# Performance work log

Hardware: AMD Instinct MI355X
Metric: run time of the kernel (lower is better)

Reference implementation:

```python
import jax, jax.numpy as jnp
import numpy as np

B, C, H, W = 2, 512, 64, 64
NUM_GROUPS = 32
EPS = 1e-6


def setup_inputs() -> dict:
    key = jax.random.key(0)
    ks = jax.random.split(key, 6)
    s = 1.0 / np.sqrt(C)
    return {
        "x": jax.random.normal(ks[0], (B, C, H, W), dtype=jnp.float32),
        "gn_scale": jnp.ones((C,), jnp.float32),
        "gn_bias": jnp.zeros((C,), jnp.float32),
        "wq": jax.random.normal(ks[1], (C, C), jnp.float32) * s,
        "bq": jnp.zeros((C,), jnp.float32),
        "wk": jax.random.normal(ks[2], (C, C), jnp.float32) * s,
        "bk": jnp.zeros((C,), jnp.float32),
        "wv": jax.random.normal(ks[3], (C, C), jnp.float32) * s,
        "bv": jnp.zeros((C,), jnp.float32),
        "wp": jax.random.normal(ks[4], (C, C), jnp.float32) * s,
        "bp": jnp.zeros((C,), jnp.float32),
    }


def group_norm(x, scale, bias):
    # x: [b, c, h, w]; GroupNorm with NUM_GROUPS groups, eps=1e-6, affine
    b, c, h, w = x.shape
    xg = x.reshape(b, NUM_GROUPS, c // NUM_GROUPS, h, w)
    mean = jnp.mean(xg, axis=(2, 3, 4), keepdims=True)
    var = jnp.var(xg, axis=(2, 3, 4), keepdims=True)
    xg = (xg - mean) * jax.lax.rsqrt(var + EPS)
    xn = xg.reshape(b, c, h, w)
    return xn * scale[None, :, None, None] + bias[None, :, None, None]


def reference(x, gn_scale, gn_bias, wq, bq, wk, bk, wv, bv, wp, bp):
    b, c, h, w = x.shape
    n = h * w
    hn = group_norm(x, gn_scale, gn_bias).reshape(b, c, n)  # [b,c,n]
    # 1x1 convs == per-pixel linear over channels
    q = jnp.einsum('dc,bcn->bdn', wq, hn) + bq[None, :, None]
    k = jnp.einsum('dc,bcn->bdn', wk, hn) + bk[None, :, None]
    v = jnp.einsum('dc,bcn->bdn', wv, hn) + bv[None, :, None]
    # attn[b,i,j] = softmax_j( q[:, :, i] . k[:, :, j] / sqrt(c) )
    attn = jnp.einsum('bci,bcj->bij', q, k) * (float(c) ** -0.5)
    attn = jax.nn.softmax(attn, axis=-1)
    out = jnp.einsum('bcj,bij->bci', v, attn)  # [b,c,n]
    out = jnp.einsum('dc,bcn->bdn', wp, out) + bp[None, :, None]
    return x + out.reshape(b, c, h, w)
```

## Files before the change

### kernel.cpp

```cpp
#include <hip/hip_runtime.h>

typedef __bf16 bf16x8 __attribute__((ext_vector_type(8)));
typedef float f32x4 __attribute__((ext_vector_type(4)));
typedef int i32x8 __attribute__((ext_vector_type(8)));
typedef _Float16 h8 __attribute__((ext_vector_type(8)));


#if defined(__has_builtin)
#if __has_builtin(__builtin_amdgcn_global_load_lds)
#define HAS_GLL 1
#endif
#endif

__device__ __forceinline__ void async_copy16(const void* g, void* l) {
#ifdef HAS_GLL
    __builtin_amdgcn_global_load_lds(
        (const __attribute__((address_space(1))) unsigned int*)g,
        (__attribute__((address_space(3))) unsigned int*)l, 16, 0, 0);
#else
    *(int4*)l = *(const int4*)g;
#endif
}

__device__ __forceinline__ unsigned char to_fp8(float v) {
    return (unsigned char)(__builtin_amdgcn_cvt_pk_fp8_f32(v, v, 0, false) & 0xFF);
}

#define MXSCALE 0x7F7F7F7F

__global__ __launch_bounds__(256) void gn_partial_kernel(const float* __restrict__ x,
                                                         float* __restrict__ ps) {
    int blk = blockIdx.x;
    const float4* base = (const float4*)x + (size_t)blk * 1024;
    float s1 = 0.f, s2 = 0.f;
#pragma unroll
    for (int i = 0; i < 4; ++i) {
        float4 v = base[threadIdx.x + (i << 8)];
        s1 += v.x + v.y + v.z + v.w;
        s2 += v.x * v.x + v.y * v.y + v.z * v.z + v.w * v.w;
    }
    for (int off = 32; off >= 1; off >>= 1) {
        s1 += __shfl_xor(s1, off);
        s2 += __shfl_xor(s2, off);
    }
    __shared__ float r1[4], r2[4];
    int wave = threadIdx.x >> 6, lane = threadIdx.x & 63;
    if (lane == 0) { r1[wave] = s1; r2[wave] = s2; }
    __syncthreads();
    if (threadIdx.x == 0) {
        ps[blk] = r1[0] + r1[1] + r1[2] + r1[3];
        ps[1024 + blk] = r2[0] + r2[1] + r2[2] + r2[3];
    }
}

__global__ __launch_bounds__(256) void gn_apply_kernel(const float* __restrict__ x,
                                                       const float* __restrict__ gn_scale,
                                                       const float* __restrict__ gn_bias,
                                                       const float* __restrict__ ps,
                                                       __bf16* __restrict__ hn_t) {
    __shared__ float tile[32][33];
    int b = blockIdx.z;
    int n0 = blockIdx.x * 32, c0 = blockIdx.y * 32;
    int tx = threadIdx.x & 31, ty = threadIdx.x >> 5;
    const float* xb = x + (size_t)b * 512 * 4096;
#pragma unroll
    for (int r = 0; r < 4; ++r) {
        int c = ty + r * 8;
        tile[c][tx] = xb[(size_t)(c0 + c) * 4096 + n0 + tx];
    }
    int c = c0 + tx;
    int g = (b << 5) + (c >> 4);
    float s1 = 0.f, s2 = 0.f;
#pragma unroll
    for (int i = 0; i < 16; ++i) {
        s1 += ps[(g << 4) + i];
        s2 += ps[1024 + (g << 4) + i];
    }
    float m = s1 * (1.f / 65536.f);
    float var = s2 * (1.f / 65536.f) - m * m;
    float rs = rsqrtf(var + 1e-6f);
    float sc = gn_scale[c] * rs;
    float bi = gn_bias[c] - m * sc;
    __syncthreads();
    __bf16* outp = hn_t + (size_t)b * 4096 * 512;
#pragma unroll
    for (int r = 0; r < 4; ++r) {
        int n = ty + r * 8;
        float v = tile[tx][n];
        outp[(size_t)(n0 + n) * 512 + c] = (__bf16)(v * sc + bi);
    }
}

__global__ __launch_bounds__(256) void cast_weights_kernel(
    const float* __restrict__ wq, const float* __restrict__ wk,
    const float* __restrict__ wv, const float* __restrict__ wp,
    const float* __restrict__ bq, const float* __restrict__ bk,
    __bf16* __restrict__ wqk_b, __bf16* __restrict__ wv_b,
    __bf16* __restrict__ wp_b, float* __restrict__ bqk) {
    int idx = blockIdx.x * 256 + threadIdx.x;
    wqk_b[idx] = (__bf16)wq[idx];
    wqk_b[262144 + idx] = (__bf16)wk[idx];
    wv_b[idx] = (__bf16)wv[idx];
    wp_b[idx] = (__bf16)wp[idx];
    if (idx < 512) {
        bqk[idx] = bq[idx];
        bqk[512 + idx] = bk[idx];
    }
}

template <int BN, int OUT_MODE, int BIAS_MODE>
__global__ __launch_bounds__(256) void gemm128_kernel(
    const __bf16* __restrict__ A, int lda, long bsA,
    const __bf16* __restrict__ Bt, int ldb, long bsB,
    void* __restrict__ C, int ldc, long bsC,
    const float* __restrict__ bias,
    const float* __restrict__ resid, long bsR,
    int K, float scale) {
    constexpr int BM = 128;
    constexpr int WM = (BN == 128) ? 64 : 32;
    constexpr int WN = 64;
    constexpr int MT = WM / 16, NT = WN / 16;
    constexpr int WAVES_N = BN / WN;
    constexpr int ACH = (BM * 64) / (8 * 256);
    constexpr int BCH = (BN * 64) / (8 * 256);

    __shared__ __align__(16) __bf16 As[BM][64];
    __shared__ __align__(16) __bf16 Bs[BN][64];

    const int tid = threadIdx.x;
    const int wave = tid >> 6, lane = tid & 63;
    const int q = lane >> 4, ln = lane & 15;
    const int wm = (wave / WAVES_N) * WM;
    const int wn = (wave % WAVES_N) * WN;
    const long m0 = (long)blockIdx.y * BM, n0 = (long)blockIdx.x * BN;
    const int b = blockIdx.z;
    const __bf16* Ab = A + (long)b * bsA + m0 * lda;
    const __bf16* Bb = Bt + (long)b * bsB + n0 * ldb;

    f32x4 acc[MT][NT] = {};

    for (int k0 = 0; k0 < K; k0 += 64) {
        __syncthreads();
#pragma unroll
        for (int p = 0; p < ACH; ++p) {
            int c = (p << 8) + tid;
            int row = c >> 3, sg = (c & 7) << 3;
            async_copy16(Ab + (long)row * lda + k0 + sg, &As[0][0] + (c << 3));
        }
#pragma unroll
        for (int p = 0; p < BCH; ++p) {
            int c = (p << 8) + tid;
            int row = c >> 3, sg = (c & 7) << 3;
            async_copy16(Bb + (long)row * ldb + k0 + sg, &Bs[0][0] + (c << 3));
        }
        __syncthreads();
#pragma unroll
        for (int kk = 0; kk < 2; ++kk) {
            bf16x8 af[MT], bfr[NT];
#pragma unroll
            for (int mt = 0; mt < MT; ++mt)
                af[mt] = *(const bf16x8*)(&As[wm + mt * 16 + ln][(kk << 5) + (q << 3)]);
#pragma unroll
            for (int nt = 0; nt < NT; ++nt)
                bfr[nt] = *(const bf16x8*)(&Bs[wn + nt * 16 + ln][(kk << 5) + (q << 3)]);
#pragma unroll
            for (int mt = 0; mt < MT; ++mt)
#pragma unroll
                for (int nt = 0; nt < NT; ++nt)
                    acc[mt][nt] = __builtin_amdgcn_mfma_f32_16x16x32_bf16(
                        af[mt], bfr[nt], acc[mt][nt], 0, 0, 0);
        }
    }

#pragma unroll
    for (int mt = 0; mt < MT; ++mt) {
#pragma unroll
        for (int nt = 0; nt < NT; ++nt) {
            long col = n0 + wn + nt * 16 + ln;
#pragma unroll
            for (int r = 0; r < 4; ++r) {
                long row = m0 + wm + mt * 16 + (q << 2) + r;
                float v = acc[mt][nt][r] * scale;
                if (BIAS_MODE == 1) v += bias[row];
                if (BIAS_MODE == 2) v += bias[col];
                long off = (long)b * bsC + row * (long)ldc + col;
                if (OUT_MODE == 0) {
                    ((__bf16*)C)[off] = (__bf16)v;
                } else if (OUT_MODE == 1) {
                    ((_Float16*)C)[off] = (_Float16)v;
                } else if (OUT_MODE == 2) {
                    ((float*)C)[off] = v + resid[(long)b * bsR + row * (long)ldc + col];
                } else {
                    ((unsigned char*)C)[off] = to_fp8(v);
                }
            }
        }
    }
}

__global__ __launch_bounds__(256) void mx_s_kernel(const unsigned char* __restrict__ QK,
                                                   _Float16* __restrict__ S,
                                                   float scale) {
    __shared__ __align__(16) unsigned char As[128 * 128];
    __shared__ __align__(16) unsigned char Bs[128 * 128];
    const int tid = threadIdx.x;
    const int lane = tid & 63, wave = tid >> 6;
    const int ln = lane & 15, q = lane >> 4;
    const int wm = (wave >> 1) << 6, wn = (wave & 1) << 6;
    const int b = blockIdx.z;
    const long m0 = (long)blockIdx.y * 128, n0 = (long)blockIdx.x * 128;
    const unsigned char* Qb = QK + (long)b * 4096 * 1024 + m0 * 1024;
    const unsigned char* Kb = QK + (long)b * 4096 * 1024 + n0 * 1024 + 512;

    f32x4 acc[4][4] = {};

    for (int k0 = 0; k0 < 512; k0 += 128) {
        __syncthreads();
#pragma unroll
        for (int p = 0; p < 4; ++p) {
            int c = (p << 8) + tid;
            int row = c >> 3, sg = (c & 7) << 4;
            async_copy16(Qb + (long)row * 1024 + k0 + sg, &As[c << 4]);
            async_copy16(Kb + (long)row * 1024 + k0 + sg, &Bs[c << 4]);
        }
        __syncthreads();
        i32x8 af[4], bf[4];
#pragma unroll
        for (int t = 0; t < 4; ++t) {
            const unsigned char* ap = &As[(wm + t * 16 + ln) * 128 + (q << 5)];
            *(int4*)&af[t] = *(const int4*)ap;
            *((int4*)&af[t] + 1) = *(const int4*)(ap + 16);
            const unsigned char* bp = &Bs[(wn + t * 16 + ln) * 128 + (q << 5)];
            *(int4*)&bf[t] = *(const int4*)bp;
            *((int4*)&bf[t] + 1) = *(const int4*)(bp + 16);
        }
#pragma unroll
        for (int mt = 0; mt < 4; ++mt)
#pragma unroll
            for (int nt = 0; nt < 4; ++nt)
                acc[mt][nt] = __builtin_amdgcn_mfma_scale_f32_16x16x128_f8f6f4(
                    af[mt], bf[nt], acc[mt][nt], 0, 0, 0, MXSCALE, 0, MXSCALE);
    }

    _Float16* Sb = S + (long)b * 4096 * 4096;
#pragma unroll
    for (int mt = 0; mt < 4; ++mt) {
#pragma unroll
        for (int nt = 0; nt < 4; ++nt) {
            long col = n0 + wn + nt * 16 + ln;
#pragma unroll
            for (int r = 0; r < 4; ++r) {
                long row = m0 + wm + mt * 16 + (q << 2) + r;
                Sb[row * 4096 + col] = (_Float16)(acc[mt][nt][r] * scale);
            }
        }
    }
}

__global__ __launch_bounds__(256) void softmax_kernel(_Float16* __restrict__ S) {
    long row = blockIdx.x;
    _Float16* srow = S + (row << 12);
    int tid = threadIdx.x;
    h8 a = ((const h8*)srow)[tid];
    h8 c = ((const h8*)srow)[tid + 256];
    float v[16];
#pragma unroll
    for (int p = 0; p < 8; ++p) {
        v[p] = (float)a[p];
        v[8 + p] = (float)c[p];
    }
    float mx = -1e30f;
#pragma unroll
    for (int p = 0; p < 16; ++p) mx = fmaxf(mx, v[p]);
    for (int off = 32; off >= 1; off >>= 1) mx = fmaxf(mx, __shfl_xor(mx, off));
    __shared__ float red[4], red2[4];
    int wave = tid >> 6, lane = tid & 63;
    if (lane == 0) red[wave] = mx;
    __syncthreads();
    mx = fmaxf(fmaxf(red[0], red[1]), fmaxf(red[2], red[3]));
    float s = 0.f;
#pragma unroll
    for (int p = 0; p < 16; ++p) {
        v[p] = __expf(v[p] - mx);
        s += v[p];
    }
    for (int off = 32; off >= 1; off >>= 1) s += __shfl_xor(s, off);
    if (lane == 0) red2[wave] = s;
    __syncthreads();
    s = red2[0] + red2[1] + red2[2] + red2[3];
    float inv64 = 64.f / s;
    int w[4];
#pragma unroll
    for (int i = 0; i < 4; ++i) {
        w[i] = __builtin_amdgcn_cvt_pk_fp8_f32(v[4 * i] * inv64, v[4 * i + 1] * inv64, 0, false);
        w[i] = __builtin_amdgcn_cvt_pk_fp8_f32(v[4 * i + 2] * inv64, v[4 * i + 3] * inv64, w[i], true);
    }
    ((int2*)srow)[tid] = make_int2(w[0], w[1]);
    ((int2*)srow)[tid + 256] = make_int2(w[2], w[3]);
}

__global__ __launch_bounds__(256) void mx_pv_kernel(const unsigned char* __restrict__ P,
                                                    const unsigned char* __restrict__ V,
                                                    __bf16* __restrict__ O) {
    __shared__ __align__(16) unsigned char As[128 * 128];
    __shared__ __align__(16) unsigned char Bs[64 * 128];
    const int tid = threadIdx.x;
    const int lane = tid & 63, wave = tid >> 6;
    const int ln = lane & 15, q = lane >> 4;
    const int wm = (wave >> 1) << 6, wn = (wave & 1) << 5;
    const int b = blockIdx.x >> 5;
    const long m0 = (long)(blockIdx.x & 31) * 128;
    const long n0 = (long)blockIdx.y * 64;
    const unsigned char* Pb = P + ((long)b * 4096 + m0) * 8192;
    const unsigned char* Vb = V + ((long)b * 512 + n0) * 4096;

    f32x4 acc[4][2] = {};

    for (int k0 = 0; k0 < 4096; k0 += 128) {
        __syncthreads();
#pragma unroll
        for (int p = 0; p < 4; ++p) {
            int c = (p << 8) + tid;
            int row = c >> 3, sg = (c & 7) << 4;
            async_copy16(Pb + (long)row * 8192 + k0 + sg, &As[c << 4]);
        }
#pragma unroll
        for (int p = 0; p < 2; ++p) {
            int c = (p << 8) + tid;
            int row = c >> 3, sg = (c & 7) << 4;
            async_copy16(Vb + (long)row * 4096 + k0 + sg, &Bs[c << 4]);
        }
        __syncthreads();
        i32x8 af[4], bf[2];
#pragma unroll
        for (int t = 0; t < 4; ++t) {
            const unsigned char* ap = &As[(wm + t * 16 + ln) * 128 + (q << 5)];
            *(int4*)&af[t] = *(const int4*)ap;
            *((int4*)&af[t] + 1) = *(const int4*)(ap + 16);
        }
#pragma unroll
        for (int t = 0; t < 2; ++t) {
            const unsigned char* bp = &Bs[(wn + t * 16 + ln) * 128 + (q << 5)];
            *(int4*)&bf[t] = *(const int4*)bp;
            *((int4*)&bf[t] + 1) = *(const int4*)(bp + 16);
        }
#pragma unroll
        for (int mt = 0; mt < 4; ++mt)
#pragma unroll
            for (int nt = 0; nt < 2; ++nt)
                acc[mt][nt] = __builtin_amdgcn_mfma_scale_f32_16x16x128_f8f6f4(
                    af[mt], bf[nt], acc[mt][nt], 0, 0, 0, MXSCALE, 0, MXSCALE);
    }

    __bf16* Ob = O + (long)b * 4096 * 512;
#pragma unroll
    for (int mt = 0; mt < 4; ++mt) {
#pragma unroll
        for (int nt = 0; nt < 2; ++nt) {
            long col = n0 + wn + nt * 16 + ln;
#pragma unroll
            for (int r = 0; r < 4; ++r) {
                long row = m0 + wm + mt * 16 + (q << 2) + r;
                Ob[row * 512 + col] = (__bf16)(acc[mt][nt][r] * 0.015625f);
            }
        }
    }
}

extern "C" void kernel_launch(void* const* d_in, const int* in_sizes, int n_in,
                              void* d_out, int out_size, void* d_ws, size_t ws_size,
                              hipStream_t stream) {
    const float* x = (const float*)d_in[0];
    const float* gn_scale = (const float*)d_in[1];
    const float* gn_bias = (const float*)d_in[2];
    const float* wq = (const float*)d_in[3];
    const float* bq = (const float*)d_in[4];
    const float* wk = (const float*)d_in[5];
    const float* bk = (const float*)d_in[6];
    const float* wv = (const float*)d_in[7];
    const float* bv = (const float*)d_in[8];
    const float* wp = (const float*)d_in[9];
    const float* bp = (const float*)d_in[10];
    float* out = (float*)d_out;

    char* ws = (char*)d_ws;
    __bf16* wqk_b = (__bf16*)(ws + 0x0);
    __bf16* wv_b = (__bf16*)(ws + 0x100000);
    __bf16* wp_b = (__bf16*)(ws + 0x180000);
    float* bqk = (float*)(ws + 0x200000);
    float* psum = (float*)(ws + 0x202000);
    __bf16* hn_t = (__bf16*)(ws + 0x210000);
    unsigned char* qk8 = (unsigned char*)(ws + 0xA10000);
    unsigned char* v8 = (unsigned char*)(ws + 0x1A10000);
    __bf16* o_t = (__bf16*)(ws + 0x2210000);
    _Float16* Sbuf = (_Float16*)(ws + 0x2A10000);
    (void)ws_size;

    cast_weights_kernel<<<1024, 256, 0, stream>>>(wq, wk, wv, wp, bq, bk,
                                                  wqk_b, wv_b, wp_b, bqk);
    gn_partial_kernel<<<1024, 256, 0, stream>>>(x, psum);
    gn_apply_kernel<<<dim3(128, 16, 2), 256, 0, stream>>>(x, gn_scale, gn_bias,
                                                          psum, hn_t);

    gemm128_kernel<128, 3, 2><<<dim3(8, 32, 2), 256, 0, stream>>>(
        hn_t, 512, 4096l * 512, wqk_b, 512, 0,
        qk8, 1024, 4096l * 1024, bqk, nullptr, 0, 512, 1.f);

    gemm128_kernel<64, 3, 1><<<dim3(64, 4, 2), 256, 0, stream>>>(
        wv_b, 512, 0, hn_t, 512, 4096l * 512,
        v8, 4096, 512l * 4096, bv, nullptr, 0, 512, 1.f);

    const float attn_scale = 0.044194173824159216f;
    mx_s_kernel<<<dim3(32, 32, 2), 256, 0, stream>>>(qk8, Sbuf, attn_scale);
    softmax_kernel<<<8192, 256, 0, stream>>>(Sbuf);
    mx_pv_kernel<<<dim3(64, 8), 256, 0, stream>>>(
        (const unsigned char*)Sbuf, v8, o_t);

    gemm128_kernel<64, 2, 1><<<dim3(64, 4, 2), 256, 0, stream>>>(
        wp_b, 512, 0, o_t, 512, 4096l * 512,
        out, 4096, 512l * 4096, bp, x, 512l * 4096, 512, 1.f);
}
```

Measured before the change: 218.0 us.

## Switch QKV projections to FP8 MX MFMA and merge prep kernels

Group-norm output and the Q/K/V weights are now stored as FP8, and the QKV projection GEMMs use the scaled 16x16x128 f8f6f4 MFMA through a generic mx_gemm kernel. The same kernel also replaces the dedicated S=QK^T kernel. Weight casting is folded into the group-norm partial-sum kernel, which saves one launch. The output projection keeps bf16 in a specialised proj_kernel. This halves the bytes moved for hn and weights and doubles MFMA throughput in the projections, at the cost of extra FP8 quantisation error in Q, K and V.

Measured after the change: 201.0 us. -7.8%, faster.

```diff
diff --git a/kernel.cpp b/kernel.cpp
--- a/kernel.cpp
+++ b/kernel.cpp
@@ -28,8 +28,25 @@
 
 #define MXSCALE 0x7F7F7F7F
 
-__global__ __launch_bounds__(256) void gn_partial_kernel(const float* __restrict__ x,
-                                                         float* __restrict__ ps) {
+__global__ __launch_bounds__(256) void prep_kernel(
+    const float* __restrict__ x, float* __restrict__ ps,
+    const float* __restrict__ wq, const float* __restrict__ wk,
+    const float* __restrict__ wv, const float* __restrict__ wp,
+    const float* __restrict__ bq, const float* __restrict__ bk,
+    unsigned char* __restrict__ wqk8, unsigned char* __restrict__ wv8,
+    __bf16* __restrict__ wp_b, float* __restrict__ bqk) {
+    if (blockIdx.x >= 1024) {
+        int idx = (blockIdx.x - 1024) * 256 + threadIdx.x;
+        wqk8[idx] = to_fp8(wq[idx]);
+        wqk8[262144 + idx] = to_fp8(wk[idx]);
+        wv8[idx] = to_fp8(wv[idx]);
+        wp_b[idx] = (__bf16)wp[idx];
+        if (idx < 512) {
+            bqk[idx] = bq[idx];
+            bqk[512 + idx] = bk[idx];
+        }
+        return;
+    }
     int blk = blockIdx.x;
     const float4* base = (const float4*)x + (size_t)blk * 1024;
     float s1 = 0.f, s2 = 0.f;
@@ -57,7 +74,7 @@
                                                        const float* __restrict__ gn_scale,
                                                        const float* __restrict__ gn_bias,
                                                        const float* __restrict__ ps,
-                                                       __bf16* __restrict__ hn_t) {
+                                                       unsigned char* __restrict__ hn8) {
     __shared__ float tile[32][33];
     int b = blockIdx.z;
     int n0 = blockIdx.x * 32, c0 = blockIdx.y * 32;
@@ -82,98 +99,74 @@
     float sc = gn_scale[c] * rs;
     float bi = gn_bias[c] - m * sc;
     __syncthreads();
-    __bf16* outp = hn_t + (size_t)b * 4096 * 512;
+    unsigned char* outp = hn8 + (size_t)b * 4096 * 512;
 #pragma unroll
     for (int r = 0; r < 4; ++r) {
         int n = ty + r * 8;
         float v = tile[tx][n];
-        outp[(size_t)(n0 + n) * 512 + c] = (__bf16)(v * sc + bi);
-    }
-}
-
-__global__ __launch_bounds__(256) void cast_weights_kernel(
-    const float* __restrict__ wq, const float* __restrict__ wk,
-    const float* __restrict__ wv, const float* __restrict__ wp,
-    const float* __restrict__ bq, const float* __restrict__ bk,
-    __bf16* __restrict__ wqk_b, __bf16* __restrict__ wv_b,
-    __bf16* __restrict__ wp_b, float* __restrict__ bqk) {
-    int idx = blockIdx.x * 256 + threadIdx.x;
-    wqk_b[idx] = (__bf16)wq[idx];
-    wqk_b[262144 + idx] = (__bf16)wk[idx];
-    wv_b[idx] = (__bf16)wv[idx];
-    wp_b[idx] = (__bf16)wp[idx];
-    if (idx < 512) {
-        bqk[idx] = bq[idx];
-        bqk[512 + idx] = bk[idx];
+        outp[(size_t)(n0 + n) * 512 + c] = to_fp8(v * sc + bi);
     }
 }
 
 template <int BN, int OUT_MODE, int BIAS_MODE>
-__global__ __launch_bounds__(256) void gemm128_kernel(
-    const __bf16* __restrict__ A, int lda, long bsA,
-    const __bf16* __restrict__ Bt, int ldb, long bsB,
+__global__ __launch_bounds__(256) void mx_gemm_kernel(
+    const unsigned char* __restrict__ A, int lda, long bsA,
+    const unsigned char* __restrict__ Bt, int ldb, long bsB,
     void* __restrict__ C, int ldc, long bsC,
-    const float* __restrict__ bias,
-    const float* __restrict__ resid, long bsR,
-    int K, float scale) {
-    constexpr int BM = 128;
-    constexpr int WM = (BN == 128) ? 64 : 32;
-    constexpr int WN = 64;
-    constexpr int MT = WM / 16, NT = WN / 16;
-    constexpr int WAVES_N = BN / WN;
-    constexpr int ACH = (BM * 64) / (8 * 256);
-    constexpr int BCH = (BN * 64) / (8 * 256);
-
-    __shared__ __align__(16) __bf16 As[BM][64];
-    __shared__ __align__(16) __bf16 Bs[BN][64];
-
+    const float* __restrict__ bias, int K, float scale) {
+    constexpr int NT = BN / 32;
+    __shared__ __align__(16) unsigned char As[128 * 128];
+    __shared__ __align__(16) unsigned char Bs[BN * 128];
     const int tid = threadIdx.x;
-    const int wave = tid >> 6, lane = tid & 63;
-    const int q = lane >> 4, ln = lane & 15;
-    const int wm = (wave / WAVES_N) * WM;
-    const int wn = (wave % WAVES_N) * WN;
-    const long m0 = (long)blockIdx.y * BM, n0 = (long)blockIdx.x * BN;
+    const int lane = tid & 63, wave = tid >> 6;
+    const int ln = lane & 15, q = lane >> 4;
+    const int wm = (wave >> 1) << 6;
+    const int wn = (wave & 1) * (BN / 2);
     const int b = blockIdx.z;
-    const __bf16* Ab = A + (long)b * bsA + m0 * lda;
-    const __bf16* Bb = Bt + (long)b * bsB + n0 * ldb;
-
-    f32x4 acc[MT][NT] = {};
-
-    for (int k0 = 0; k0 < K; k0 += 64) {
-        __syncthreads();
-#pragma unroll
-        for (int p = 0; p < ACH; ++p) {
-            int c = (p << 8) + tid;
-            int row = c >> 3, sg = (c & 7) << 3;
-            async_copy16(Ab + (long)row * lda + k0 + sg, &As[0][0] + (c << 3));
-        }
-#pragma unroll
-        for (int p = 0; p < BCH; ++p) {
-            int c = (p << 8) + tid;
-            int row = c >> 3, sg = (c & 7) << 3;
-            async_copy16(Bb + (long)row * ldb + k0 + sg, &Bs[0][0] + (c << 3));
-        }
-        __syncthreads();
-#pragma unroll
-        for (int kk = 0; kk < 2; ++kk) {
-            bf16x8 af[MT], bfr[NT];
-#pragma unroll
-            for (int mt = 0; mt < MT; ++mt)
-                af[mt] = *(const bf16x8*)(&As[wm + mt * 16 + ln][(kk << 5) + (q << 3)]);
+    const long m0 = (long)blockIdx.y * 128, n0 = (long)blockIdx.x * BN;
+    const unsigned char* Ab = A + (long)b * bsA + m0 * lda;
+    const unsigned char* Bb = Bt + (long)b * bsB + n0 * ldb;
+
+    f32x4 acc[4][NT] = {};
+
+    for (int k0 = 0; k0 < K; k0 += 128) {
+        __syncthreads();
+#pragma unroll
+        for (int p = 0; p < 4; ++p) {
+            int c = (p << 8) + tid;
+            int row = c >> 3, sg = (c & 7) << 4;
+            async_copy16(Ab + (long)row * lda + k0 + sg, &As[c << 4]);
+        }
+#pragma unroll
+        for (int p = 0; p < BN / 32; ++p) {
+            int c = (p << 8) + tid;
+            int row = c >> 3, sg = (c & 7) << 4;
+            async_copy16(Bb + (long)row * ldb + k0 + sg, &Bs[c << 4]);
+        }
+        __syncthreads();
+        i32x8 af[4], bf[NT];
+#pragma unroll
+        for (int t = 0; t < 4; ++t) {
+            const unsigned char* ap = &As[(wm + t * 16 + ln) * 128 + (q << 5)];
+            *(int4*)&af[t] = *(const int4*)ap;
+            *((int4*)&af[t] + 1) = *(const int4*)(ap + 16);
+        }
+#pragma unroll
+        for (int t = 0; t < NT; ++t) {
+            const unsigned char* bp = &Bs[(wn + t * 16 + ln) * 128 + (q << 5)];
+            *(int4*)&bf[t] = *(const int4*)bp;
+            *((int4*)&bf[t] + 1) = *(const int4*)(bp + 16);
+        }
+#pragma unroll
+        for (int mt = 0; mt < 4; ++mt)
 #pragma unroll
             for (int nt = 0; nt < NT; ++nt)
-                bfr[nt] = *(const bf16x8*)(&Bs[wn + nt * 16 + ln][(kk << 5) + (q << 3)]);
-#pragma unroll
-            for (int mt = 0; mt < MT; ++mt)
-#pragma unroll
-                for (int nt = 0; nt < NT; ++nt)
-                    acc[mt][nt] = __builtin_amdgcn_mfma_f32_16x16x32_bf16(
-                        af[mt], bfr[nt], acc[mt][nt], 0, 0, 0);
-        }
-    }
-
-#pragma unroll
-    for (int mt = 0; mt < MT; ++mt) {
+                acc[mt][nt] = __builtin_amdgcn_mfma_scale_f32_16x16x128_f8f6f4(
+                    af[mt], bf[nt], acc[mt][nt], 0, 0, 0, MXSCALE, 0, MXSCALE);
+    }
+
+#pragma unroll
+    for (int mt = 0; mt < 4; ++mt) {
 #pragma unroll
         for (int nt = 0; nt < NT; ++nt) {
             long col = n0 + wn + nt * 16 + ln;
@@ -185,73 +178,10 @@
                 if (BIAS_MODE == 2) v += bias[col];
                 long off = (long)b * bsC + row * (long)ldc + col;
                 if (OUT_MODE == 0) {
-                    ((__bf16*)C)[off] = (__bf16)v;
-                } else if (OUT_MODE == 1) {
+                    ((unsigned char*)C)[off] = to_fp8(v);
+                } else {
                     ((_Float16*)C)[off] = (_Float16)v;
-                } else if (OUT_MODE == 2) {
-                    ((float*)C)[off] = v + resid[(long)b * bsR + row * (long)ldc + col];
-                } else {
-                    ((unsigned char*)C)[off] = to_fp8(v);
                 }
-            }
-        }
-    }
-}
-
-__global__ __launch_bounds__(256) void mx_s_kernel(const unsigned char* __restrict__ QK,
-                                                   _Float16* __restrict__ S,
-                                                   float scale) {
-    __shared__ __align__(16) unsigned char As[128 * 128];
-    __shared__ __align__(16) unsigned char Bs[128 * 128];
-    const int tid = threadIdx.x;
-    const int lane = tid & 63, wave = tid >> 6;
-    const int ln = lane & 15, q = lane >> 4;
-    const int wm = (wave >> 1) << 6, wn = (wave & 1) << 6;
-    const int b = blockIdx.z;
-    const long m0 = (long)blockIdx.y * 128, n0 = (long)blockIdx.x * 128;
-    const unsigned char* Qb = QK + (long)b * 4096 * 1024 + m0 * 1024;
-    const unsigned char* Kb = QK + (long)b * 4096 * 1024 + n0 * 1024 + 512;
-
-    f32x4 acc[4][4] = {};
-
-    for (int k0 = 0; k0 < 512; k0 += 128) {
-        __syncthreads();
-#pragma unroll
-        for (int p = 0; p < 4; ++p) {
-            int c = (p << 8) + tid;
-            int row = c >> 3, sg = (c & 7) << 4;
-            async_copy16(Qb + (long)row * 1024 + k0 + sg, &As[c << 4]);
-            async_copy16(Kb + (long)row * 1024 + k0 + sg, &Bs[c << 4]);
-        }
-        __syncthreads();
-        i32x8 af[4], bf[4];
-#pragma unroll
-        for (int t = 0; t < 4; ++t) {
-            const unsigned char* ap = &As[(wm + t * 16 + ln) * 128 + (q << 5)];
-            *(int4*)&af[t] = *(const int4*)ap;
-            *((int4*)&af[t] + 1) = *(const int4*)(ap + 16);
-            const unsigned char* bp = &Bs[(wn + t * 16 + ln) * 128 + (q << 5)];
-            *(int4*)&bf[t] = *(const int4*)bp;
-            *((int4*)&bf[t] + 1) = *(const int4*)(bp + 16);
-        }
-#pragma unroll
-        for (int mt = 0; mt < 4; ++mt)
-#pragma unroll
-            for (int nt = 0; nt < 4; ++nt)
-                acc[mt][nt] = __builtin_amdgcn_mfma_scale_f32_16x16x128_f8f6f4(
-                    af[mt], bf[nt], acc[mt][nt], 0, 0, 0, MXSCALE, 0, MXSCALE);
-    }
-
-    _Float16* Sb = S + (long)b * 4096 * 4096;
-#pragma unroll
-    for (int mt = 0; mt < 4; ++mt) {
-#pragma unroll
-        for (int nt = 0; nt < 4; ++nt) {
-            long col = n0 + wn + nt * 16 + ln;
-#pragma unroll
-            for (int r = 0; r < 4; ++r) {
-                long row = m0 + wm + mt * 16 + (q << 2) + r;
-                Sb[row * 4096 + col] = (_Float16)(acc[mt][nt][r] * scale);
             }
         }
     }
@@ -362,6 +292,71 @@
             for (int r = 0; r < 4; ++r) {
                 long row = m0 + wm + mt * 16 + (q << 2) + r;
                 Ob[row * 512 + col] = (__bf16)(acc[mt][nt][r] * 0.015625f);
+            }
+        }
+    }
+}
+
+__global__ __launch_bounds__(256) void proj_kernel(
+    const __bf16* __restrict__ A, const __bf16* __restrict__ Bt, long bsB,
+    float* __restrict__ C, long bsC, const float* __restrict__ bias,
+    const float* __restrict__ resid) {
+    __shared__ __align__(16) __bf16 As[128][64];
+    __shared__ __align__(16) __bf16 Bs[64][64];
+    const int tid = threadIdx.x;
+    const int wave = tid >> 6, lane = tid & 63;
+    const int q = lane >> 4, ln = lane & 15;
+    const int wm = wave << 5;
+    const long m0 = (long)blockIdx.y * 128, n0 = (long)blockIdx.x * 64;
+    const int b = blockIdx.z;
+    const __bf16* Ab = A + m0 * 512;
+    const __bf16* Bb = Bt + (long)b * bsB + n0 * 512;
+
+    f32x4 acc[2][4] = {};
+
+    for (int k0 = 0; k0 < 512; k0 += 64) {
+        __syncthreads();
+#pragma unroll
+        for (int p = 0; p < 4; ++p) {
+            int c = (p << 8) + tid;
+            int row = c >> 3, sg = (c & 7) << 3;
+            async_copy16(Ab + (long)row * 512 + k0 + sg, &As[0][0] + (c << 3));
+        }
+#pragma unroll
+        for (int p = 0; p < 2; ++p) {
+            int c = (p << 8) + tid;
+            int row = c >> 3, sg = (c & 7) << 3;
+            async_copy16(Bb + (long)row * 512 + k0 + sg, &Bs[0][0] + (c << 3));
+        }
+        __syncthreads();
+#pragma unroll
+        for (int kk = 0; kk < 2; ++kk) {
+            bf16x8 af[2], bfr[4];
+#pragma unroll
+            for (int mt = 0; mt < 2; ++mt)
+                af[mt] = *(const bf16x8*)(&As[wm + mt * 16 + ln][(kk << 5) + (q << 3)]);
+#pragma unroll
+            for (int nt = 0; nt < 4; ++nt)
+                bfr[nt] = *(const bf16x8*)(&Bs[nt * 16 + ln][(kk << 5) + (q << 3)]);
+#pragma unroll
+            for (int mt = 0; mt < 2; ++mt)
+#pragma unroll
+                for (int nt = 0; nt < 4; ++nt)
+                    acc[mt][nt] = __builtin_amdgcn_mfma_f32_16x16x32_bf16(
+                        af[mt], bfr[nt], acc[mt][nt], 0, 0, 0);
+        }
+    }
+
+#pragma unroll
+    for (int mt = 0; mt < 2; ++mt) {
+#pragma unroll
+        for (int nt = 0; nt < 4; ++nt) {
+            long col = n0 + nt * 16 + ln;
+#pragma unroll
+            for (int r = 0; r < 4; ++r) {
+                long row = m0 + wm + mt * 16 + (q << 2) + r;
+                long off = (long)b * bsC + row * 4096 + col;
+                C[off] = acc[mt][nt][r] + bias[row] + resid[off];
             }
         }
     }
@@ -384,39 +379,39 @@
     float* out = (float*)d_out;
 
     char* ws = (char*)d_ws;
-    __bf16* wqk_b = (__bf16*)(ws + 0x0);
-    __bf16* wv_b = (__bf16*)(ws + 0x100000);
-    __bf16* wp_b = (__bf16*)(ws + 0x180000);
-    float* bqk = (float*)(ws + 0x200000);
-    float* psum = (float*)(ws + 0x202000);
-    __bf16* hn_t = (__bf16*)(ws + 0x210000);
-    unsigned char* qk8 = (unsigned char*)(ws + 0xA10000);
-    unsigned char* v8 = (unsigned char*)(ws + 0x1A10000);
-    __bf16* o_t = (__bf16*)(ws + 0x2210000);
-    _Float16* Sbuf = (_Float16*)(ws + 0x2A10000);
+    unsigned char* wqk8 = (unsigned char*)(ws + 0x0);
+    unsigned char* wv8 = (unsigned char*)(ws + 0x80000);
+    __bf16* wp_b = (__bf16*)(ws + 0xC0000);
+    float* bqk = (float*)(ws + 0x140000);
+    float* psum = (float*)(ws + 0x142000);
+    unsigned char* hn8 = (unsigned char*)(ws + 0x150000);
+    unsigned char* qk8 = (unsigned char*)(ws + 0x550000);
+    unsigned char* v8 = (unsigned char*)(ws + 0xD50000);
+    __bf16* o_t = (__bf16*)(ws + 0x1150000);
+    _Float16* Sbuf = (_Float16*)(ws + 0x1950000);
     (void)ws_size;
 
-    cast_weights_kernel<<<1024, 256, 0, stream>>>(wq, wk, wv, wp, bq, bk,
-                                                  wqk_b, wv_b, wp_b, bqk);
-    gn_partial_kernel<<<1024, 256, 0, stream>>>(x, psum);
+    prep_kernel<<<2048, 256, 0, stream>>>(x, psum, wq, wk, wv, wp, bq, bk,
+                                          wqk8, wv8, wp_b, bqk);
     gn_apply_kernel<<<dim3(128, 16, 2), 256, 0, stream>>>(x, gn_scale, gn_bias,
-                                                          psum, hn_t);
-
-    gemm128_kernel<128, 3, 2><<<dim3(8, 32, 2), 256, 0, stream>>>(
-        hn_t, 512, 4096l * 512, wqk_b, 512, 0,
-        qk8, 1024, 4096l * 1024, bqk, nullptr, 0, 512, 1.f);
-
-    gemm128_kernel<64, 3, 1><<<dim3(64, 4, 2), 256, 0, stream>>>(
-        wv_b, 512, 0, hn_t, 512, 4096l * 512,
-        v8, 4096, 512l * 4096, bv, nullptr, 0, 512, 1.f);
+                                                          psum, hn8);
+
+    mx_gemm_kernel<128, 0, 2><<<dim3(8, 32, 2), 256, 0, stream>>>(
+        hn8, 512, 4096l * 512, wqk8, 512, 0,
+        qk8, 1024, 4096l * 1024, bqk, 512, 1.f);
+
+    mx_gemm_kernel<64, 0, 1><<<dim3(64, 4, 2), 256, 0, stream>>>(
+        wv8, 512, 0, hn8, 512, 4096l * 512,
+        v8, 4096, 512l * 4096, bv, 512, 1.f);
 
     const float attn_scale = 0.044194173824159216f;
-    mx_s_kernel<<<dim3(32, 32, 2), 256, 0, stream>>>(qk8, Sbuf, attn_scale);
+    mx_gemm_kernel<128, 1, 0><<<dim3(32, 32, 2), 256, 0, stream>>>(
+        qk8, 1024, 4096l * 1024, qk8 + 512, 1024, 4096l * 1024,
+        Sbuf, 4096, 4096l * 4096, nullptr, 512, attn_scale);
     softmax_kernel<<<8192, 256, 0, stream>>>(Sbuf);
     mx_pv_kernel<<<dim3(64, 8), 256, 0, stream>>>(
         (const unsigned char*)Sbuf, v8, o_t);
 
-    gemm128_kernel<64, 2, 1><<<dim3(64, 4, 2), 256, 0, stream>>>(
-        wp_b, 512, 0, o_t, 512, 4096l * 512,
-        out, 4096, 512l * 4096, bp, x, 512l * 4096, 512, 1.f);
-}
+    proj_kernel<<<dim3(64, 4, 2), 256, 0, stream>>>(
+        wp_b, o_t, 4096l * 512, out, 512l * 4096, bp, x);
+}
```
